# Kernel tuning notes

Measured on AMD Instinct MI355X. Metric: run time of the kernel, lower is better.

Reference implementation:

```python
import jax, jax.numpy as jnp
import numpy as np

EMB_DIM = 1024
N_HEADS = 16
HEAD_DIM = EMB_DIM // N_HEADS


def setup_inputs() -> dict:
    key = jax.random.key(0)
    ks = jax.random.split(key, 6)
    B, T, C = 2, 2048, EMB_DIM
    s = 1.0 / np.sqrt(C)
    return {
        "x": jax.random.normal(ks[0], (B, T, C), dtype=jnp.float32),
        "W_query": jax.random.normal(ks[1], (C, C), dtype=jnp.float32) * s,
        "W_key": jax.random.normal(ks[2], (C, C), dtype=jnp.float32) * s,
        "W_value": jax.random.normal(ks[3], (C, C), dtype=jnp.float32) * s,
        "W_out": jax.random.normal(ks[4], (C, C), dtype=jnp.float32) * s,
        "b_out": jax.random.normal(ks[5], (C,), dtype=jnp.float32) * 0.01,
    }


def reference(x, W_query, W_key, W_value, W_out, b_out):
    # x: [B, T, C]. Linear weights stored as [in, out] (transposed torch layout).
    B, T, C = x.shape
    H, D = N_HEADS, HEAD_DIM

    def split_heads(t):  # [B,T,C] -> [B,H,T,D]
        return t.reshape(B, T, H, D).transpose(0, 2, 1, 3)

    q = split_heads(x @ W_query)
    k = split_heads(x @ W_key)
    v = split_heads(x @ W_value)

    scale = 1.0 / jnp.sqrt(jnp.asarray(D, dtype=x.dtype))
    att = jnp.einsum("bhqd,bhkd->bhqk", q, k) * scale  # [B,H,T,T]
    causal = jnp.tril(jnp.ones((T, T), dtype=bool))
    att = jnp.where(causal[None, None], att, jnp.asarray(-jnp.inf, dtype=att.dtype))
    att = jax.nn.softmax(att, axis=-1)
    # dropout is identity in eval / drop_rate=0
    y = jnp.einsum("bhqk,bhkd->bhqd", att, v)  # [B,H,T,D]
    y = y.transpose(0, 2, 1, 3).reshape(B, T, C)
    return y @ W_out + b_out
```

## Files before the change

kernel.cpp:

```cpp
#include <hip/hip_runtime.h>
#include <hip/hip_bf16.h>
#include <math.h>

#define Bsz 2
#define Tsz 2048
#define Csz 1024
#define Hsz 16
#define Dsz 64

typedef __attribute__((ext_vector_type(8))) short frag8;
typedef __attribute__((ext_vector_type(4))) float f4;
typedef __attribute__((ext_vector_type(8))) unsigned short us8;
typedef __attribute__((ext_vector_type(4))) _Float16 frag4h;
typedef __attribute__((ext_vector_type(8))) _Float16 frag8h;

static __device__ __forceinline__ unsigned short f2bf(float f) {
  union { __hip_bfloat16 h; unsigned short u; } c;
  c.h = __float2bfloat16(f);
  return c.u;
}
static __device__ __forceinline__ unsigned short f2h(float f) {
  union { _Float16 h; unsigned short u; } c;
  c.h = (_Float16)f;
  return c.u;
}

#define GLDS16(g, l)                                                        \
  __builtin_amdgcn_global_load_lds(                                         \
      (const __attribute__((address_space(1))) void*)(g),                   \
      (__attribute__((address_space(3))) void*)(l), 16, 0, 0)

#define QSCALE 0.18033688f

__global__ __launch_bounds__(256) void cast_x(const float* __restrict__ x,
                                              unsigned short* __restrict__ xb) {
  const int i = (blockIdx.x * 256 + threadIdx.x) * 8;
  const float4 a = *(const float4*)(x + i);
  const float4 b = *(const float4*)(x + i + 4);
  us8 v;
  v[0] = f2bf(a.x); v[1] = f2bf(a.y); v[2] = f2bf(a.z); v[3] = f2bf(a.w);
  v[4] = f2bf(b.x); v[5] = f2bf(b.y); v[6] = f2bf(b.z); v[7] = f2bf(b.w);
  *(us8*)(xb + i) = v;
}

__global__ __launch_bounds__(256) void transpose_cast(
    const float* __restrict__ s0, const float* __restrict__ s1,
    const float* __restrict__ s2, const float* __restrict__ s3,
    unsigned short* __restrict__ d0, unsigned short* __restrict__ d1,
    unsigned short* __restrict__ d2, unsigned short* __restrict__ d3) {
  __shared__ float Ls[64][65];
  const int mat = blockIdx.x >> 8;
  const int tile = blockIdx.x & 255;
  const float* src = mat == 0 ? s0 : mat == 1 ? s1 : mat == 2 ? s2 : s3;
  unsigned short* dst = mat == 0 ? d0 : mat == 1 ? d1 : mat == 2 ? d2 : d3;
  const int tr0 = (tile >> 4) << 6, tc0 = (tile & 15) << 6;
  const int t = threadIdx.x;
  const int lr = t >> 4, lc = (t & 15) << 2;
#pragma unroll
  for (int j = 0; j < 4; ++j) {
    const float4 v = *(const float4*)(src + (size_t)(tr0 + lr + j * 16) * 1024 + tc0 + lc);
    Ls[lr + j * 16][lc + 0] = v.x;
    Ls[lr + j * 16][lc + 1] = v.y;
    Ls[lr + j * 16][lc + 2] = v.z;
    Ls[lr + j * 16][lc + 3] = v.w;
  }
  __syncthreads();
#pragma unroll
  for (int j = 0; j < 4; ++j) {
    ushort4 v;
    v.x = f2bf(Ls[lc + 0][lr + j * 16]);
    v.y = f2bf(Ls[lc + 1][lr + j * 16]);
    v.z = f2bf(Ls[lc + 2][lr + j * 16]);
    v.w = f2bf(Ls[lc + 3][lr + j * 16]);
    *(ushort4*)(dst + (size_t)(tc0 + lr + j * 16) * 1024 + tr0 + lc) = v;
  }
}

template <int MODE, int MT>
__global__ __launch_bounds__(256) void mm_bt(
    const unsigned short* __restrict__ A, const unsigned short* __restrict__ Bt,
    const float* __restrict__ bias, unsigned short* __restrict__ O0,
    unsigned short* __restrict__ O1, unsigned short* __restrict__ O2,
    float* __restrict__ Of) {
  __shared__ __align__(16) unsigned short As[MT * 32 * 64];
  __shared__ __align__(16) unsigned short Bs[128 * 64];
  const int K = 1024;
  const int tid = threadIdx.x;
  const int wave = tid >> 6, lane = tid & 63;
  const int quad = lane >> 4, l16 = lane & 15;
  const int wrow = (wave >> 1) * (MT * 16), wn = wave & 1;
  const int row0 = blockIdx.y * (MT * 32), col0 = blockIdx.x << 7;

  const int sr = lane >> 3, sg = lane & 7;
  const int g0 = sg ^ sr;
  const unsigned short* gA = A + (size_t)(row0 + wave * (MT * 8) + sr) * K + (g0 << 3);
  const unsigned short* gB = Bt + (size_t)(col0 + wave * 32 + sr) * K + (g0 << 3);

  f4 acc[MT][4];
#pragma unroll
  for (int i = 0; i < MT; ++i)
#pragma unroll
    for (int j = 0; j < 4; ++j) acc[i][j] = (f4){0.f, 0.f, 0.f, 0.f};

  for (int kk = 0; kk < K; kk += 64) {
    __syncthreads();
#pragma unroll
    for (int s = 0; s < MT; ++s)
      GLDS16(gA + kk + (size_t)(s * 8) * K, &As[(wave * (MT * 8) + s * 8) * 64]);
#pragma unroll
    for (int s = 0; s < 4; ++s)
      GLDS16(gB + kk + (size_t)(s * 8) * K, &Bs[(wave * 32 + s * 8) * 64]);
    __syncthreads();

#pragma unroll
    for (int ks = 0; ks < 2; ++ks) {
      frag8 af[MT], bf[4];
#pragma unroll
      for (int mt = 0; mt < MT; ++mt) {
        const int r = wrow + mt * 16 + l16;
        af[mt] = *(const frag8*)&As[r * 64 + (((ks * 4 + quad) ^ (l16 & 7)) << 3)];
      }
#pragma unroll
      for (int nt = 0; nt < 4; ++nt) {
        const int n = wn * 64 + nt * 16 + l16;
        bf[nt] = *(const frag8*)&Bs[n * 64 + (((ks * 4 + quad) ^ (l16 & 7)) << 3)];
      }
#pragma unroll
      for (int mt = 0; mt < MT; ++mt)
#pragma unroll
        for (int nt = 0; nt < 4; ++nt)
          acc[mt][nt] = __builtin_amdgcn_mfma_f32_16x16x32_bf16(af[mt], bf[nt], acc[mt][nt], 0, 0, 0);
    }
  }

  if (MODE == 0) {
    if (col0 < 2048) {
      const bool isK = (col0 >= 1024);
      unsigned short* dst = isK ? O1 : O0;
      const float sc = isK ? 1.0f : QSCALE;
#pragma unroll
      for (int mt = 0; mt < MT; ++mt)
#pragma unroll
        for (int nt = 0; nt < 4; ++nt) {
          const int m = row0 + wrow + mt * 16 + quad * 4;
          const int n = (col0 & 1023) + wn * 64 + nt * 16 + l16;
          const int b = m >> 11, h = n >> 6, d = n & 63;
#pragma unroll
          for (int r = 0; r < 4; ++r) {
            const int tk = (m + r) & (Tsz - 1);
            dst[(((size_t)b * Hsz + h) * Tsz + tk) * Dsz + d] = f2bf(acc[mt][nt][r] * sc);
          }
        }
    } else {
#pragma unroll
      for (int mt = 0; mt < MT; ++mt)
#pragma unroll
        for (int nt = 0; nt < 4; ++nt) {
          const int tok = row0 + wrow + mt * 16 + quad * 4;
          const int ch = (col0 - 2048) + wn * 64 + nt * 16 + l16;
          const int b = tok >> 11, tk = tok & (Tsz - 1);
          const int h = ch >> 6, d = ch & 63;
          const int t5 = tk & 31;
          const int pos = (tk & ~31) + ((t5 >> 4) << 2) + (((t5 >> 2) & 3) << 3) + (t5 & 3);
          ushort4 v;
          v.x = f2h(acc[mt][nt][0]); v.y = f2h(acc[mt][nt][1]);
          v.z = f2h(acc[mt][nt][2]); v.w = f2h(acc[mt][nt][3]);
          *(ushort4*)&O2[(((size_t)b * Hsz + h) * Dsz + d) * Tsz + pos] = v;
        }
    }
  } else {
#pragma unroll
    for (int mt = 0; mt < MT; ++mt)
#pragma unroll
      for (int nt = 0; nt < 4; ++nt) {
        const int m = row0 + wrow + mt * 16 + quad * 4;
        const int n = col0 + wn * 64 + nt * 16 + l16;
        const float bv = bias[n];
#pragma unroll
        for (int r = 0; r < 4; ++r)
          Of[(size_t)(m + r) * Csz + n] = acc[mt][nt][r] + bv;
      }
  }
}

__global__ __launch_bounds__(512, 4) void attn_mfma(
    const unsigned short* __restrict__ Qb,
    const unsigned short* __restrict__ Kb,
    const unsigned short* __restrict__ VTb,
    unsigned short* __restrict__ Y) {
  __shared__ __align__(16) unsigned char SMEM[65536];
#define KSP(spp, bb) ((unsigned short*)(SMEM + (spp) * 16384 + (bb) * 4096))
#define VSP(spp, bb) ((unsigned short*)(SMEM + (spp) * 16384 + 8192 + (bb) * 4096))

  const int tid = threadIdx.x;
  const int wave = tid >> 6, lane = tid & 63;
  const int quad = lane >> 4, l16 = lane & 15;
  const int t = wave & 1;
  const int sp = wave >> 1;
  const int ltid = tid & 127;

  const int bh = blockIdx.x & 31;
  const int pr = blockIdx.x >> 5;
  const int ja = pr, jb = 63 - pr;
  const int qa0 = ja << 5, qb0 = jb << 5;

  const unsigned short* Qh = Qb + (size_t)bh * Tsz * Dsz;
  const unsigned short* Kh = Kb + (size_t)bh * Tsz * Dsz;
  const unsigned short* Vh = VTb + (size_t)bh * Dsz * Tsz;

  const int ke0 = ltid, ke1 = ltid + 128;
  const int kkey0 = ke0 >> 3, kc0 = ke0 & 7;
  const int kkey1 = ke1 >> 3, kc1 = ke1 & 7;
  const unsigned short* gK0 = Kh + (size_t)kkey0 * Dsz + ((kc0 ^ (kkey0 & 7)) << 3);
  const unsigned short* gK1 = Kh + (size_t)kkey1 * Dsz + ((kc1 ^ (kkey1 & 7)) << 3);
  const int vd0 = ltid >> 2, vc0 = ltid & 3;
  const int vd1 = vd0 + 32;
  const unsigned short* gV0 = Vh + (size_t)vd0 * Tsz + ((vc0 ^ ((vd0 + (vd0 >> 2)) & 3)) << 3);
  const unsigned short* gV1 = Vh + (size_t)vd1 * Tsz + ((vc0 ^ ((vd1 + (vd1 >> 2)) & 3)) << 3);
  const int wo = t * 512;

  frag8 qfa[2], qfb[2];
#pragma unroll
  for (int ks = 0; ks < 2; ++ks) {
    qfa[ks] = *(const frag8*)(Qh + (size_t)(qa0 + t * 16 + l16) * Dsz + ks * 32 + quad * 8);
    qfb[ks] = *(const frag8*)(Qh + (size_t)(qb0 + t * 16 + l16) * Dsz + ks * 32 + quad * 8);
  }

  f4 oa[4], ob[4];
  float lsa = 0.f, lsb = 0.f;
#pragma unroll
  for (int nt = 0; nt < 4; ++nt) {
    oa[nt] = (f4){0.f, 0.f, 0.f, 0.f};
    ob[nt] = (f4){0.f, 0.f, 0.f, 0.f};
  }
  const f4 zf = (f4){0.f, 0.f, 0.f, 0.f};
  const int fl = (l16 + (l16 >> 2)) & 3;
  const int qq = t * 16 + l16;

  const int nch = (jb >> 2) + 1;

  {
    const size_t kof0 = (size_t)(sp << 5) * Dsz, kof1 = (size_t)((sp + 4) << 5) * Dsz;
    const int vof0 = sp << 5, vof1 = (sp + 4) << 5;
    GLDS16(gK0 + kof0, KSP(sp, 0) + wo);
    GLDS16(gK1 + kof0, KSP(sp, 0) + wo + 1024);
    GLDS16(gV0 + vof0, VSP(sp, 0) + wo);
    GLDS16(gV1 + vof0, VSP(sp, 0) + wo + 1024);
    GLDS16(gK0 + kof1, KSP(sp, 1) + wo);
    GLDS16(gK1 + kof1, KSP(sp, 1) + wo + 1024);
    GLDS16(gV0 + vof1, VSP(sp, 1) + wo);
    GLDS16(gV1 + vof1, VSP(sp, 1) + wo + 1024);
  }
  __syncthreads();

  for (int i = 0; i < nch; ++i) {
    const int c = sp + 4 * i;
    const int bsel = i & 1;
    if (c <= jb) {
      const unsigned short* Kl = KSP(sp, bsel);
      const unsigned short* Vl = VSP(sp, bsel);
      frag8 kf[2][2];
#pragma unroll
      for (int n = 0; n < 2; ++n)
#pragma unroll
        for (int ks = 0; ks < 2; ++ks)
          kf[n][ks] = *(const frag8*)&Kl[(n * 16 + l16) * 64 + (((ks * 4 + quad) ^ (l16 & 7)) << 3)];
      frag8h vf[4];
#pragma unroll
      for (int nt = 0; nt < 4; ++nt)
        vf[nt] = *(const frag8h*)&Vl[(nt * 16 + l16) * 32 + ((quad ^ fl) << 3)];

      {
        f4 st[2];
#pragma unroll
        for (int n = 0; n < 2; ++n) {
          f4 a = __builtin_amdgcn_mfma_f32_16x16x32_bf16(kf[n][0], qfb[0], zf, 0, 0, 0);
          st[n] = __builtin_amdgcn_mfma_f32_16x16x32_bf16(kf[n][1], qfb[1], a, 0, 0, 0);
        }
        const bool dm = (c == jb);
        frag4h paf[2];
#pragma unroll
        for (int n = 0; n < 2; ++n) {
          const int key0 = n * 16 + quad * 4;
          float p[4];
#pragma unroll
          for (int r = 0; r < 4; ++r) {
            float sv = st[n][r];
            if (dm && (key0 + r > qq)) sv = -INFINITY;
            p[r] = __builtin_amdgcn_exp2f(sv);
          }
          lsb += (p[0] + p[1]) + (p[2] + p[3]);
          frag4h ph;
          ph[0] = (_Float16)p[0]; ph[1] = (_Float16)p[1];
          ph[2] = (_Float16)p[2]; ph[3] = (_Float16)p[3];
          paf[n] = ph;
        }
#pragma unroll
        for (int nt = 0; nt < 4; ++nt) {
          const frag4h vlo = __builtin_shufflevector(vf[nt], vf[nt], 0, 1, 2, 3);
          const frag4h vhi = __builtin_shufflevector(vf[nt], vf[nt], 4, 5, 6, 7);
          f4 a = __builtin_amdgcn_mfma_f32_16x16x16f16(paf[0], vlo, ob[nt], 0, 0, 0);
          ob[nt] = __builtin_amdgcn_mfma_f32_16x16x16f16(paf[1], vhi, a, 0, 0, 0);
        }
      }
      if (c <= ja) {
        f4 st[2];
#pragma unroll
        for (int n = 0; n < 2; ++n) {
          f4 a = __builtin_amdgcn_mfma_f32_16x16x32_bf16(kf[n][0], qfa[0], zf, 0, 0, 0);
          st[n] = __builtin_amdgcn_mfma_f32_16x16x32_bf16(kf[n][1], qfa[1], a, 0, 0, 0);
        }
        const bool dm = (c == ja);
        frag4h paf[2];
#pragma unroll
        for (int n = 0; n < 2; ++n) {
          const int key0 = n * 16 + quad * 4;
          float p[4];
#pragma unroll
          for (int r = 0; r < 4; ++r) {
            float sv = st[n][r];
            if (dm && (key0 + r > qq)) sv = -INFINITY;
            p[r] = __builtin_amdgcn_exp2f(sv);
          }
          lsa += (p[0] + p[1]) + (p[2] + p[3]);
          frag4h ph;
          ph[0] = (_Float16)p[0]; ph[1] = (_Float16)p[1];
          ph[2] = (_Float16)p[2]; ph[3] = (_Float16)p[3];
          paf[n] = ph;
        }
#pragma unroll
        for (int nt = 0; nt < 4; ++nt) {
          const frag4h vlo = __builtin_shufflevector(vf[nt], vf[nt], 0, 1, 2, 3);
          const frag4h vhi = __builtin_shufflevector(vf[nt], vf[nt], 4, 5, 6, 7);
          f4 a = __builtin_amdgcn_mfma_f32_16x16x16f16(paf[0], vlo, oa[nt], 0, 0, 0);
          oa[nt] = __builtin_amdgcn_mfma_f32_16x16x16f16(paf[1], vhi, a, 0, 0, 0);
        }
      }
    }
    __syncthreads();
    if (i + 2 < nch) {
      const int c2 = sp + 4 * (i + 2);
      const size_t kof = (size_t)(c2 << 5) * Dsz;
      const int vof = c2 << 5;
      GLDS16(gK0 + kof, KSP(sp, bsel) + wo);
      GLDS16(gK1 + kof, KSP(sp, bsel) + wo + 1024);
      GLDS16(gV0 + vof, VSP(sp, bsel) + wo);
      GLDS16(gV1 + vof, VSP(sp, bsel) + wo + 1024);
    }
  }

  float* comb = (float*)SMEM;
  const int slot = (sp - 1) * 2 + t;
  float* cp = comb + (size_t)(slot * 64 + lane) * 37;
  if (sp != 0) {
#pragma unroll
    for (int nt = 0; nt < 4; ++nt) {
      *(f4*)(cp + nt * 4) = oa[nt];
      *(f4*)(cp + 16 + nt * 4) = ob[nt];
    }
    cp[32] = lsa; cp[33] = lsb;
  }
  __syncthreads();
  if (sp == 0) {
#pragma unroll
    for (int s = 0; s < 3; ++s) {
      const float* rp = comb + (size_t)((s * 2 + t) * 64 + lane) * 37;
#pragma unroll
      for (int nt = 0; nt < 4; ++nt) {
        oa[nt] += *(const f4*)(rp + nt * 4);
        ob[nt] += *(const f4*)(rp + 16 + nt * 4);
      }
      lsa += rp[32]; lsb += rp[33];
    }

    lsa += __shfl_xor(lsa, 16); lsa += __shfl_xor(lsa, 32);
    lsb += __shfl_xor(lsb, 16); lsb += __shfl_xor(lsb, 32);
    const int b = bh >> 4, h = bh & 15;
#pragma unroll
    for (int r = 0; r < 4; ++r) {
      const float inv = 1.f / __shfl(lsa, quad * 4 + r);
      const int tk = qa0 + t * 16 + quad * 4 + r;
      unsigned short* yp = Y + ((size_t)b * Tsz + tk) * Csz + h * 64 + l16;
#pragma unroll
      for (int nt = 0; nt < 4; ++nt)
        yp[nt * 16] = f2bf(oa[nt][r] * inv);
    }
#pragma unroll
    for (int r = 0; r < 4; ++r) {
      const float inv = 1.f / __shfl(lsb, quad * 4 + r);
      const int tk = qb0 + t * 16 + quad * 4 + r;
      unsigned short* yp = Y + ((size_t)b * Tsz + tk) * Csz + h * 64 + l16;
#pragma unroll
      for (int nt = 0; nt < 4; ++nt)
        yp[nt * 16] = f2bf(ob[nt][r] * inv);
    }
  }
#undef KSP
#undef VSP
}

extern "C" void kernel_launch(void* const* d_in, const int* in_sizes, int n_in,
                              void* d_out, int out_size, void* d_ws, size_t ws_size,
                              hipStream_t stream) {
  const float* x  = (const float*)d_in[0];
  const float* Wq = (const float*)d_in[1];
  const float* Wk = (const float*)d_in[2];
  const float* Wv = (const float*)d_in[3];
  const float* Wo = (const float*)d_in[4];
  const float* bo = (const float*)d_in[5];

  const size_t NEL = (size_t)Bsz * Tsz * Csz;
  const size_t WSZ = (size_t)Csz * Csz;
  unsigned short* xb  = (unsigned short*)d_ws;
  unsigned short* WT  = xb + NEL;
  unsigned short* WoT = WT + 3 * WSZ;
  unsigned short* Qb  = WoT + WSZ;
  unsigned short* Kb  = Qb + NEL;
  unsigned short* VTb = Kb + NEL;
  unsigned short* Yb  = VTb + NEL;

  cast_x<<<NEL / 2048, 256, 0, stream>>>(x, xb);
  transpose_cast<<<1024, 256, 0, stream>>>(Wq, Wk, Wv, Wo,
                                           WT, WT + WSZ, WT + 2 * WSZ, WoT);

  mm_bt<0, 4><<<dim3(24, 32), 256, 0, stream>>>(xb, WT, nullptr, Qb, Kb, VTb, nullptr);

  attn_mfma<<<1024, 512, 0, stream>>>(Qb, Kb, VTb, Yb);

  mm_bt<2, 2><<<dim3(8, 64), 256, 0, stream>>>(Yb, WoT, bo, nullptr, nullptr, nullptr,
                                               (float*)d_out);
}
```

Baseline: 180.7 us.

## Restructure attention K/V double-buffer pipeline with partial vmcnt waits

Replaces the full __syncthreads before each chunk with a partial s_waitcnt vmcnt(4) plus barrier, so the previous chunk's async global-to-LDS loads can stay in flight. K/V fragments are read from LDS into registers first, then the next stage load is issued right away, before the MFMA compute instead of after it. This gives more overlap between memory and compute. A dummy reload of the last chunk keeps the outstanding-load count constant so the fixed vmcnt stays valid. The cost is redundant loads and extra barriers on iterations where the chunk is skipped.

```diff
diff --git a/kernel.cpp b/kernel.cpp
--- a/kernel.cpp
+++ b/kernel.cpp
@@ -225,6 +225,7 @@
     qfa[ks] = *(const frag8*)(Qh + (size_t)(qa0 + t * 16 + l16) * Dsz + ks * 32 + quad * 8);
     qfb[ks] = *(const frag8*)(Qh + (size_t)(qb0 + t * 16 + l16) * Dsz + ks * 32 + quad * 8);
   }
+  asm volatile("s_waitcnt vmcnt(0)" ::: "memory");
 
   f4 oa[4], ob[4];
   float lsa = 0.f, lsb = 0.f;
@@ -238,38 +239,48 @@
   const int qq = t * 16 + l16;
 
   const int nch = (jb >> 2) + 1;
-
-  {
-    const size_t kof0 = (size_t)(sp << 5) * Dsz, kof1 = (size_t)((sp + 4) << 5) * Dsz;
-    const int vof0 = sp << 5, vof1 = (sp + 4) << 5;
-    GLDS16(gK0 + kof0, KSP(sp, 0) + wo);
-    GLDS16(gK1 + kof0, KSP(sp, 0) + wo + 1024);
-    GLDS16(gV0 + vof0, VSP(sp, 0) + wo);
-    GLDS16(gV1 + vof0, VSP(sp, 0) + wo + 1024);
-    GLDS16(gK0 + kof1, KSP(sp, 1) + wo);
-    GLDS16(gK1 + kof1, KSP(sp, 1) + wo + 1024);
-    GLDS16(gV0 + vof1, VSP(sp, 1) + wo);
-    GLDS16(gV1 + vof1, VSP(sp, 1) + wo + 1024);
-  }
-  __syncthreads();
+  const int clast = sp + ((nch - 1) << 2);
+
+  auto STAGE = [&](int bb, int cc) {
+    const size_t kof = (size_t)(cc << 5) * Dsz;
+    const int vof = cc << 5;
+    GLDS16(gK0 + kof, KSP(sp, bb) + wo);
+    GLDS16(gK1 + kof, KSP(sp, bb) + wo + 1024);
+    GLDS16(gV0 + vof, VSP(sp, bb) + wo);
+    GLDS16(gV1 + vof, VSP(sp, bb) + wo + 1024);
+  };
+
+  STAGE(0, sp);
+  STAGE(1, sp + 4);
 
   for (int i = 0; i < nch; ++i) {
     const int c = sp + 4 * i;
     const int bsel = i & 1;
+
+    asm volatile("s_waitcnt vmcnt(4)" ::: "memory");
+    __builtin_amdgcn_s_barrier();
+    __builtin_amdgcn_sched_barrier(0);
+
+    const unsigned short* Kl = KSP(sp, bsel);
+    const unsigned short* Vl = VSP(sp, bsel);
+    frag8 kf[2][2];
+#pragma unroll
+    for (int n = 0; n < 2; ++n)
+#pragma unroll
+      for (int ks = 0; ks < 2; ++ks)
+        kf[n][ks] = *(const frag8*)&Kl[(n * 16 + l16) * 64 + (((ks * 4 + quad) ^ (l16 & 7)) << 3)];
+    frag8h vf[4];
+#pragma unroll
+    for (int nt = 0; nt < 4; ++nt)
+      vf[nt] = *(const frag8h*)&Vl[(nt * 16 + l16) * 32 + ((quad ^ fl) << 3)];
+
+    asm volatile("s_waitcnt lgkmcnt(0)" ::: "memory");
+    __builtin_amdgcn_s_barrier();
+    __builtin_amdgcn_sched_barrier(0);
+
+    STAGE(bsel, (i + 2 < nch) ? c + 8 : clast);
+
     if (c <= jb) {
-      const unsigned short* Kl = KSP(sp, bsel);
-      const unsigned short* Vl = VSP(sp, bsel);
-      frag8 kf[2][2];
-#pragma unroll
-      for (int n = 0; n < 2; ++n)
-#pragma unroll
-        for (int ks = 0; ks < 2; ++ks)
-          kf[n][ks] = *(const frag8*)&Kl[(n * 16 + l16) * 64 + (((ks * 4 + quad) ^ (l16 & 7)) << 3)];
-      frag8h vf[4];
-#pragma unroll
-      for (int nt = 0; nt < 4; ++nt)
-        vf[nt] = *(const frag8h*)&Vl[(nt * 16 + l16) * 32 + ((quad ^ fl) << 3)];
-
       {
         f4 st[2];
 #pragma unroll
@@ -337,18 +348,9 @@
         }
       }
     }
-    __syncthreads();
-    if (i + 2 < nch) {
-      const int c2 = sp + 4 * (i + 2);
-      const size_t kof = (size_t)(c2 << 5) * Dsz;
-      const int vof = c2 << 5;
-      GLDS16(gK0 + kof, KSP(sp, bsel) + wo);
-      GLDS16(gK1 + kof, KSP(sp, bsel) + wo + 1024);
-      GLDS16(gV0 + vof, VSP(sp, bsel) + wo);
-      GLDS16(gV1 + vof, VSP(sp, bsel) + wo + 1024);
-    }
-  }
-
+  }
+
+  __syncthreads();
   float* comb = (float*)SMEM;
   const int slot = (sp - 1) * 2 + t;
   float* cp = comb + (size_t)(slot * 64 + lane) * 37;
```

Result: slower. 184.5 us (+2.1%).
